# Kernel tuning notes

Hardware: AMD Instinct MI355X
Metric: run time of the kernel (lower is better)

Reference implementation:

```python
import jax, jax.numpy as jnp
import numpy as np

T, B, V, L_MAX = 1000, 64, 1024, 64
BLANK = 0
LAMBDA_FAIR = 0.5
NUM_GROUPS = 2
NEG = jnp.float32(-1e30)  # finite stand-in for -inf (nan-safe under vjp)


def setup_inputs() -> dict:
    key = jax.random.key(0)
    k1, k2, k3, k4, k5 = jax.random.split(key, 5)
    # caller passes log-softmaxed acoustic model outputs [T, B, V]
    log_probs = jax.nn.log_softmax(jax.random.normal(k1, (T, B, V), jnp.float32), axis=-1)
    # flat concatenated targets; values in [1, V) (blank=0 excluded, as in real CTC targets)
    targets = jax.random.randint(k2, (B * L_MAX,), 1, V, dtype=jnp.int32)
    input_lengths = jax.random.randint(k3, (B,), T // 2, T + 1, dtype=jnp.int32)
    target_lengths = jax.random.randint(k4, (B,), 0, L_MAX, dtype=jnp.int32)  # 0 allowed (tests t_len==0 branch)
    group_ids = jax.random.randint(k5, (B,), 0, NUM_GROUPS, dtype=jnp.int32)
    return {"log_probs": log_probs, "targets": targets, "input_lengths": input_lengths,
            "target_lengths": target_lengths, "group_ids": group_ids}


def _ctc_per_sample(log_probs, targets, input_lengths, target_lengths):
    """Batched CTC NLL (reduction='none'), log-domain alpha recursion."""
    Tn, Bn, Vn = log_probs.shape
    # unflatten targets per sample: offsets = exclusive cumsum of target_lengths
    offsets = jnp.cumsum(target_lengths) - target_lengths                      # [B]
    pos = offsets[:, None] + jnp.arange(L_MAX)[None, :]                        # [B, L]
    valid = jnp.arange(L_MAX)[None, :] < target_lengths[:, None]
    tgt = jnp.where(valid, targets[jnp.clip(pos, 0, targets.shape[0] - 1)], BLANK)  # [B, L]

    S = 2 * L_MAX + 1  # extended label sequence with interleaved blanks
    ext = jnp.full((Bn, S), BLANK, dtype=targets.dtype).at[:, 1::2].set(tgt)   # [B, S]
    # emission log-probs gathered once: em[t, b, s] = log_probs[t, b, ext[b, s]]
    em = jnp.take_along_axis(log_probs, jnp.broadcast_to(ext[None], (Tn, Bn, S)), axis=2)

    ext_m2 = jnp.pad(ext[:, :-2], ((0, 0), (2, 0)), constant_values=BLANK)
    s_idx = jnp.arange(S)
    allow_skip = (s_idx[None, :] >= 2) & (ext != BLANK) & (ext != ext_m2)      # [B, S]

    def end_ll(alpha):
        last = 2 * target_lengths                                              # index of final blank
        a1 = jnp.take_along_axis(alpha, last[:, None], axis=1)[:, 0]
        a2 = jnp.take_along_axis(alpha, jnp.clip(last - 1, 0)[:, None], axis=1)[:, 0]
        return jnp.logaddexp(a1, jnp.where(target_lengths > 0, a2, NEG))

    alpha0 = jnp.full((Bn, S), NEG).at[:, 0].set(em[0, :, 0])
    alpha0 = alpha0.at[:, 1].set(jnp.where(target_lengths > 0, em[0, :, 1], NEG))
    final0 = jnp.where(input_lengths == 1, end_ll(alpha0), NEG)

    def step(carry, xs):
        alpha, final = carry
        em_t, t = xs
        sh1 = jnp.concatenate([jnp.full((Bn, 1), NEG), alpha[:, :-1]], axis=1)
        sh2 = jnp.concatenate([jnp.full((Bn, 2), NEG), alpha[:, :-2]], axis=1)
        alpha = jnp.logaddexp(jnp.logaddexp(alpha, sh1),
                              jnp.where(allow_skip, sh2, NEG)) + em_t
        final = jnp.where(t == input_lengths - 1, end_ll(alpha), final)
        return (alpha, final), None

    (_, final), _ = jax.lax.scan(step, (alpha0, final0), (em[1:], jnp.arange(1, Tn)))
    loss = jnp.where(target_lengths > 0, -final, 0.0)   # t_len==0 -> loss 0 (as in original)
    loss = jnp.where(loss < 1e29, loss, 0.0)            # zero_infinity=True
    return loss


def reference(log_probs, targets, input_lengths, target_lengths, group_ids):
    per_sample = _ctc_per_sample(log_probs, targets, input_lengths, target_lengths)  # [B]
    base_loss = per_sample.mean()
    ones = jnp.ones_like(per_sample)
    counts = jax.ops.segment_sum(ones, group_ids, num_segments=NUM_GROUPS)
    sums = jax.ops.segment_sum(per_sample, group_ids, num_segments=NUM_GROUPS)
    group_means = sums / jnp.maximum(counts, 1.0)
    fairness_penalty = jnp.var(group_means, ddof=1)     # torch .var() is unbiased
    total = base_loss + LAMBDA_FAIR * fairness_penalty
    return total, base_loss, fairness_penalty
```

## Files before the change

kernel.cpp:

```cpp
#include <hip/hip_runtime.h>

#define T_ 1000
#define B_ 64
#define V_ 1024
#define LMAX_ 64
#define NEGF (-1e30f)
#define LOG2E_ 1.4426950408889634f
#define LN2_ 0.6931471805599453f
#define P0C 1.4405f
#define P1C (-0.64178f)
#define P2C 0.20128f

__device__ __forceinline__ float ex2(float x) { return __builtin_amdgcn_exp2f(x); }
__device__ __forceinline__ float lg2(float x) { return __builtin_amdgcn_logf(x); }
__device__ __forceinline__ float rlane(float x, int l) {
    return __int_as_float(__builtin_amdgcn_readlane(__float_as_int(x), l));
}
#define FENCE_ __builtin_amdgcn_sched_barrier(0)

__device__ __forceinline__ void load_tgt(const int* __restrict__ targets,
                                         const int* __restrict__ tlen,
                                         int b, int lane, int& tg, int& L) {
    int tl = tlen[lane];
    L = __shfl(tl, b);
    int v = (lane < b) ? tl : 0;
    for (int off = 32; off; off >>= 1) v += __shfl_xor(v, off);
    tg = (lane < L) ? targets[v + lane] : 0;
}

__global__ __launch_bounds__(64) void ctc_fb_k(const float* __restrict__ lp,
                                               const int* __restrict__ targets,
                                               const int* __restrict__ tlen,
                                               const int* __restrict__ ilen,
                                               float* __restrict__ aw) {
    int blk = blockIdx.x, lane = threadIdx.x;
    bool isFwd = blk < B_;
    int b = isFwd ? blk : blk - B_;
    int tg, L;
    load_tgt(targets, tlen, b, lane, tg, L);
    int Tin = ilen[b], Te = Tin - 1;
    int M = Te >> 1;
    int tgp = __shfl_up(tg, 1);
    bool skip1 = (lane >= 1) && (tg != 0) && (tg != tgp);
    int col = (lane == 63) ? 0 : tg;
    int idx = (b << 10) + col;
    float* awb = aw + b * 256;

    if (isFwd) {
        bool is16 = (lane == 16), is32 = (lane == 32), is48 = (lane == 48);
        float a0 = NEGF, a1 = NEGF;
        auto ldG = [&](int g, float4& S) {
            int t0 = 4 * g;
            int ta = t0 < M ? t0 : M, tb2 = t0 + 1 < M ? t0 + 1 : M;
            int tc = t0 + 2 < M ? t0 + 2 : M, td = t0 + 3 < M ? t0 + 3 : M;
            S.x = (lp + ((size_t)ta << 16))[idx];
            S.y = (lp + ((size_t)tb2 << 16))[idx];
            S.z = (lp + ((size_t)tc << 16))[idx];
            S.w = (lp + ((size_t)td << 16))[idx];
        };
        auto shr1 = [&](float x) -> float {
            float v15 = rlane(x, 15), v31 = rlane(x, 31), v47 = rlane(x, 47);
            float bval = is16 ? v15 : (is32 ? v31 : (is48 ? v47 : NEGF));
            return __int_as_float(__builtin_amdgcn_update_dpp(
                __float_as_int(bval), __float_as_int(x), 0x111, 0xF, 0xF, false));
        };
        auto step = [&](float xb, float xe) {
            float p1m = shr1(a1);
            float d0 = a0 - p1m;
            float m0 = fmaxf(a0, p1m);
            float u = ex2(-fabsf(d0));
            float h = fmaf(u, P2C, P1C);
            h = fmaf(u, h, P0C);
            float U = fmaf(u, h, m0);
            float na0 = U + xb;
            float w = skip1 ? U : a0;
            float d1 = a1 - w;
            float m1 = fmaxf(a1, w);
            float v = ex2(-fabsf(d1));
            float h1 = fmaf(v, P2C, P1C);
            h1 = fmaf(v, h1, P0C);
            float na1 = fmaf(v, h1, m1 + xe);
            a0 = na0; a1 = na1;
        };
        if (M >= 35) {
            float4 S0, S1, S2, S3, S4, S5, S6, S7;
            ldG(0, S0); ldG(1, S1); ldG(2, S2); ldG(3, S3);
            ldG(4, S4); ldG(5, S5); ldG(6, S6); ldG(7, S7);
            FENCE_;
            {
                float e0 = S0.x * LOG2E_, e1 = S0.y * LOG2E_;
                float e2 = S0.z * LOG2E_, e3 = S0.w * LOG2E_;
                a0 = (lane == 0) ? rlane(e0, 63) : NEGF;
                a1 = (lane == 0 && L > 0) ? e0 : NEGF;
                step(rlane(e1, 63), e1); step(rlane(e2, 63), e2); step(rlane(e3, 63), e3);
                ldG(8, S0);
                FENCE_;
            }
#define SUBF_F(S, G) do {                                                      \
            float e0_ = S.x * LOG2E_, e1_ = S.y * LOG2E_;                      \
            float e2_ = S.z * LOG2E_, e3_ = S.w * LOG2E_;                      \
            float b0_ = rlane(e0_, 63), b1_ = rlane(e1_, 63);                  \
            float b2_ = rlane(e2_, 63), b3_ = rlane(e3_, 63);                  \
            step(b0_, e0_); step(b1_, e1_); step(b2_, e2_); step(b3_, e3_);    \
            ldG((G) + 8, S);                                                   \
            FENCE_;                                                            \
        } while (0)
            SUBF_F(S1, 1); SUBF_F(S2, 2); SUBF_F(S3, 3); SUBF_F(S4, 4);
            SUBF_F(S5, 5); SUBF_F(S6, 6); SUBF_F(S7, 7);
            int c = 1;
            for (; 32 * c + 31 <= M; ++c) {
                int g0 = 8 * c;
                SUBF_F(S0, g0 + 0); SUBF_F(S1, g0 + 1); SUBF_F(S2, g0 + 2); SUBF_F(S3, g0 + 3);
                SUBF_F(S4, g0 + 4); SUBF_F(S5, g0 + 5); SUBF_F(S6, g0 + 6); SUBF_F(S7, g0 + 7);
            }
#undef SUBF_F
            int tb = 32 * c;
#define SUBT_F(S, T0) do {                                                     \
            float e0_ = S.x * LOG2E_, e1_ = S.y * LOG2E_;                      \
            float e2_ = S.z * LOG2E_, e3_ = S.w * LOG2E_;                      \
            float b0_ = rlane(e0_, 63), b1_ = rlane(e1_, 63);                  \
            float b2_ = rlane(e2_, 63), b3_ = rlane(e3_, 63);                  \
            if ((T0) + 0 <= M) step(b0_, e0_);                                 \
            if ((T0) + 1 <= M) step(b1_, e1_);                                 \
            if ((T0) + 2 <= M) step(b2_, e2_);                                 \
            if ((T0) + 3 <= M) step(b3_, e3_);                                 \
        } while (0)
            SUBT_F(S0, tb + 0);  SUBT_F(S1, tb + 4);  SUBT_F(S2, tb + 8);  SUBT_F(S3, tb + 12);
            SUBT_F(S4, tb + 16); SUBT_F(S5, tb + 20); SUBT_F(S6, tb + 24); SUBT_F(S7, tb + 28);
#undef SUBT_F
        } else {
            float e = lp[idx] * LOG2E_;
            a0 = (lane == 0) ? rlane(e, 63) : NEGF;
            a1 = (lane == 0 && L > 0) ? e : NEGF;
            for (int t = 1; t <= M; ++t) {
                float xe = (lp + ((size_t)t << 16))[idx] * LOG2E_;
                step(rlane(xe, 63), xe);
            }
        }
        awb[lane] = a0;
        awb[64 + lane] = a1;
    } else {
        bool is15 = (lane == 15), is31 = (lane == 31), is47 = (lane == 47);
        int K = Te - M;
        float B0 = (lane == L) ? 0.0f : NEGF;
        float B1 = (L > 0 && lane == L - 1) ? 0.0f : NEGF;
        auto ldG = [&](int g, float4& S) {
            int t0 = Te - 4 * g;
            int ta = t0 > 0 ? t0 : 0, tb2 = t0 - 1 > 0 ? t0 - 1 : 0;
            int tc = t0 - 2 > 0 ? t0 - 2 : 0, td = t0 - 3 > 0 ? t0 - 3 : 0;
            S.x = (lp + ((size_t)ta << 16))[idx];
            S.y = (lp + ((size_t)tb2 << 16))[idx];
            S.z = (lp + ((size_t)tc << 16))[idx];
            S.w = (lp + ((size_t)td << 16))[idx];
        };
        auto shl1 = [&](float x) -> float {
            float v16 = rlane(x, 16), v32 = rlane(x, 32), v48 = rlane(x, 48);
            float bval = is15 ? v16 : (is31 ? v32 : (is47 ? v48 : NEGF));
            return __int_as_float(__builtin_amdgcn_update_dpp(
                __float_as_int(bval), __float_as_int(x), 0x101, 0xF, 0xF, false));
        };
        auto stepb = [&](float xb, float xe) {
            float z = B1 + xe;
            float t0v = B0 + xb;
            float d0 = t0v - z;
            float m0 = fmaxf(t0v, z);
            float u = ex2(-fabsf(d0));
            float h = fmaf(u, P2C, P1C);
            h = fmaf(u, h, P0C);
            float B0n = fmaf(u, h, m0);
            float y = skip1 ? B0n : t0v;
            float arg = shl1(y);
            float d1 = z - arg;
            float m1 = fmaxf(z, arg);
            float v = ex2(-fabsf(d1));
            float h1 = fmaf(v, P2C, P1C);
            h1 = fmaf(v, h1, P0C);
            float B1n = fmaf(v, h1, m1);
            B0 = B0n; B1 = B1n;
        };
        if (K >= 35) {
            float4 S0, S1, S2, S3, S4, S5, S6, S7;
            ldG(0, S0); ldG(1, S1); ldG(2, S2); ldG(3, S3);
            ldG(4, S4); ldG(5, S5); ldG(6, S6); ldG(7, S7);
            FENCE_;
#define SUBF_B(S, G) do {                                                      \
            float e0_ = S.x * LOG2E_, e1_ = S.y * LOG2E_;                      \
            float e2_ = S.z * LOG2E_, e3_ = S.w * LOG2E_;                      \
            float b0_ = rlane(e0_, 63), b1_ = rlane(e1_, 63);                  \
            float b2_ = rlane(e2_, 63), b3_ = rlane(e3_, 63);                  \
            stepb(b0_, e0_); stepb(b1_, e1_); stepb(b2_, e2_); stepb(b3_, e3_);\
            ldG((G) + 8, S);                                                   \
            FENCE_;                                                            \
        } while (0)
            SUBF_B(S0, 0); SUBF_B(S1, 1); SUBF_B(S2, 2); SUBF_B(S3, 3);
            SUBF_B(S4, 4); SUBF_B(S5, 5); SUBF_B(S6, 6); SUBF_B(S7, 7);
            int c = 1;
            for (; 32 * c + 31 <= K - 1; ++c) {
                int g0 = 8 * c;
                SUBF_B(S0, g0 + 0); SUBF_B(S1, g0 + 1); SUBF_B(S2, g0 + 2); SUBF_B(S3, g0 + 3);
                SUBF_B(S4, g0 + 4); SUBF_B(S5, g0 + 5); SUBF_B(S6, g0 + 6); SUBF_B(S7, g0 + 7);
            }
#undef SUBF_B
            int kb = 32 * c;
#define SUBT_B(S, K0) do {                                                     \
            float e0_ = S.x * LOG2E_, e1_ = S.y * LOG2E_;                      \
            float e2_ = S.z * LOG2E_, e3_ = S.w * LOG2E_;                      \
            float b0_ = rlane(e0_, 63), b1_ = rlane(e1_, 63);                  \
            float b2_ = rlane(e2_, 63), b3_ = rlane(e3_, 63);                  \
            if ((K0) + 0 <= K - 1) stepb(b0_, e0_);                            \
            if ((K0) + 1 <= K - 1) stepb(b1_, e1_);                            \
            if ((K0) + 2 <= K - 1) stepb(b2_, e2_);                            \
            if ((K0) + 3 <= K - 1) stepb(b3_, e3_);                            \
        } while (0)
            SUBT_B(S0, kb + 0);  SUBT_B(S1, kb + 4);  SUBT_B(S2, kb + 8);  SUBT_B(S3, kb + 12);
            SUBT_B(S4, kb + 16); SUBT_B(S5, kb + 20); SUBT_B(S6, kb + 24); SUBT_B(S7, kb + 28);
#undef SUBT_B
        } else {
            for (int k = 0; k < K; ++k) {
                int t = Te - k;
                float xe = (lp + ((size_t)t << 16))[idx] * LOG2E_;
                stepb(rlane(xe, 63), xe);
            }
        }
        awb[128 + lane] = B0;
        awb[192 + lane] = B1;
    }
}

__global__ __launch_bounds__(64) void combine_k(const float* __restrict__ aw,
                                                const int* __restrict__ tlen,
                                                const int* __restrict__ ilen,
                                                float* __restrict__ losses) {
    int b = blockIdx.x, lane = threadIdx.x;
    const float* awb = aw + b * 256;
    float s0 = awb[lane] + awb[128 + lane];
    float s1 = awb[64 + lane] + awb[192 + lane];
    float m = fmaxf(s0, s1);
    for (int off = 32; off; off >>= 1) m = fmaxf(m, __shfl_xor(m, off));
    float sum = ex2(s0 - m) + ex2(s1 - m);
    for (int off = 32; off; off >>= 1) sum += __shfl_xor(sum, off);
    if (lane == 0) {
        int L = tlen[b];
        float fin = lg2(sum) + m;
        if (ilen[b] <= 0) fin = NEGF;
        float loss = (L > 0) ? -fin * LN2_ : 0.0f;
        if (!(loss < 1e29f)) loss = 0.0f;
        losses[b] = loss;
    }
}

__global__ __launch_bounds__(64) void ctc_rec_direct_k(const float* __restrict__ lp,
                                                       const int* __restrict__ targets,
                                                       const int* __restrict__ tlen,
                                                       const int* __restrict__ ilen,
                                                       float* __restrict__ losses) {
    int b = blockIdx.x, lane = threadIdx.x;
    int tg, L;
    load_tgt(targets, tlen, b, lane, tg, L);
    int Tin = ilen[b], Te = Tin - 1;
    int tgp = __shfl_up(tg, 1);
    bool skip1 = (lane >= 1) && (tg != 0) && (tg != tgp);
    bool is16 = (lane == 16), is32 = (lane == 32), is48 = (lane == 48);
    int col = (lane == 63) ? 0 : tg;
    int idx = (b << 10) + col;
    float a0 = NEGF, a1 = NEGF;
    auto shr1 = [&](float x) -> float {
        float v15 = rlane(x, 15), v31 = rlane(x, 31), v47 = rlane(x, 47);
        float bval = is16 ? v15 : (is32 ? v31 : (is48 ? v47 : NEGF));
        return __int_as_float(__builtin_amdgcn_update_dpp(
            __float_as_int(bval), __float_as_int(x), 0x111, 0xF, 0xF, false));
    };
    auto step = [&](float xb, float xe) {
        float p1m = shr1(a1);
        float d0 = a0 - p1m;
        float m0 = fmaxf(a0, p1m);
        float u = ex2(-fabsf(d0));
        float h = fmaf(u, P2C, P1C);
        h = fmaf(u, h, P0C);
        float U = fmaf(u, h, m0);
        float na0 = U + xb;
        float w = skip1 ? U : a0;
        float d1 = a1 - w;
        float m1 = fmaxf(a1, w);
        float v = ex2(-fabsf(d1));
        float h1 = fmaf(v, P2C, P1C);
        h1 = fmaf(v, h1, P0C);
        float na1 = fmaf(v, h1, m1 + xe);
        a0 = na0; a1 = na1;
    };
    if (Tin >= 1) {
        float e = lp[idx] * LOG2E_;
        a0 = (lane == 0) ? rlane(e, 63) : NEGF;
        a1 = (lane == 0 && L > 0) ? e : NEGF;
        for (int t = 1; t <= Te; ++t) {
            float xe = (lp + ((size_t)t << 16))[idx] * LOG2E_;
            step(rlane(xe, 63), xe);
        }
    }
    int lidx = (L > 0) ? (L - 1) : 0;
    float aPrev = __shfl(a1, lidx);
    float aLast = __shfl(a0, (L < 63) ? L : 63);
    float x = aLast, y = (L > 0) ? aPrev : NEGF;
    float m = fmaxf(x, y), d = fminf(x, y) - m;
    float fin = m + lg2(1.0f + ex2(d));
    if (Tin <= 0) fin = NEGF;
    if (lane == 0) {
        float loss = (L > 0) ? -fin * LN2_ : 0.0f;
        if (!(loss < 1e29f)) loss = 0.0f;
        losses[b] = loss;
    }
}

__global__ __launch_bounds__(64) void finalize_k(const float* __restrict__ losses,
                                                 const int* __restrict__ gid,
                                                 float* __restrict__ out) {
    int lane = threadIdx.x;
    float l = losses[lane];
    int g = gid[lane];
    float s = l;
    float s0 = (g == 0) ? l : 0.0f, c0 = (g == 0) ? 1.0f : 0.0f;
    float s1 = (g == 1) ? l : 0.0f, c1 = (g == 1) ? 1.0f : 0.0f;
    for (int off = 32; off; off >>= 1) {
        s  += __shfl_xor(s, off);
        s0 += __shfl_xor(s0, off);
        c0 += __shfl_xor(c0, off);
        s1 += __shfl_xor(s1, off);
        c1 += __shfl_xor(c1, off);
    }
    if (lane == 0) {
        float base = s * (1.0f / B_);
        float m0 = s0 / fmaxf(c0, 1.0f);
        float m1 = s1 / fmaxf(c1, 1.0f);
        float mean = 0.5f * (m0 + m1);
        float var = (m0 - mean) * (m0 - mean) + (m1 - mean) * (m1 - mean);
        out[0] = base + 0.5f * var;
        out[1] = base;
        out[2] = var;
    }
}

extern "C" void kernel_launch(void* const* d_in, const int* in_sizes, int n_in,
                              void* d_out, int out_size, void* d_ws, size_t ws_size,
                              hipStream_t stream) {
    const float* lp = (const float*)d_in[0];
    const int* targets = (const int*)d_in[1];
    const int* ilen = (const int*)d_in[2];
    const int* tlen = (const int*)d_in[3];
    const int* gid = (const int*)d_in[4];
    float* out = (float*)d_out;

    char* ws = (char*)d_ws;
    float* losses = (float*)ws;
    float* aw = (float*)(ws + 1024);
    size_t need = 1024 + (size_t)B_ * 256 * 4;

    if (ws_size >= need) {
        ctc_fb_k<<<2 * B_, 64, 0, stream>>>(lp, targets, tlen, ilen, aw);
        combine_k<<<B_, 64, 0, stream>>>(aw, tlen, ilen, losses);
    } else {
        ctc_rec_direct_k<<<B_, 64, 0, stream>>>(lp, targets, tlen, ilen, losses);
    }
    finalize_k<<<1, 64, 0, stream>>>(losses, gid, out);
}
```

Measured before the change: 46.37 us.

## Pre-gather emissions into contiguous float4 buffer and fuse combine with finalize

Adds a highly parallel gather kernel that pulls the needed emission log-probs from the large [T,B,V] tensor, scales them to log2, and writes them into a per-sample, time-packed float4 layout. The serial forward/backward recursion kernels then read one coalesced float4 per lane per four timesteps, instead of four scattered 4-byte loads on the latency-bound critical path. The combine and finalize kernels are merged into one single-block tail kernel to save a launch. The cost is an extra kernel launch plus about 4 MB of workspace writes and reads, and the fast path now needs a larger workspace.

```diff
diff --git a/kernel.cpp b/kernel.cpp
--- a/kernel.cpp
+++ b/kernel.cpp
@@ -1,9 +1,9 @@
 #include <hip/hip_runtime.h>
 
 #define T_ 1000
+#define T4_ 250
 #define B_ 64
 #define V_ 1024
-#define LMAX_ 64
 #define NEGF (-1e30f)
 #define LOG2E_ 1.4426950408889634f
 #define LN2_ 0.6931471805599453f
@@ -28,7 +28,25 @@
     tg = (lane < L) ? targets[v + lane] : 0;
 }
 
-__global__ __launch_bounds__(64) void ctc_fb_k(const float* __restrict__ lp,
+__global__ __launch_bounds__(256) void gather_k(const float* __restrict__ lp,
+                                                const int* __restrict__ targets,
+                                                const int* __restrict__ tlen,
+                                                const int* __restrict__ ilen,
+                                                float* __restrict__ em4f) {
+    int t4 = blockIdx.x % T4_;
+    int b = blockIdx.x / T4_;
+    int tq = threadIdx.x >> 6;
+    int i = threadIdx.x & 63;
+    int tg, L;
+    load_tgt(targets, tlen, b, i, tg, L);
+    int t = t4 * 4 + tq;
+    if (t >= ilen[b]) return;
+    int col = (i == 63) ? 0 : tg;
+    em4f[(((size_t)b * T4_ + t4) * 64 + i) * 4 + tq] =
+        lp[((size_t)t << 16) + (b << 10) + col] * LOG2E_;
+}
+
+__global__ __launch_bounds__(64) void ctc_fb_k(const float4* __restrict__ e44,
                                                const int* __restrict__ targets,
                                                const int* __restrict__ tlen,
                                                const int* __restrict__ ilen,
@@ -42,21 +60,16 @@
     int M = Te >> 1;
     int tgp = __shfl_up(tg, 1);
     bool skip1 = (lane >= 1) && (tg != 0) && (tg != tgp);
-    int col = (lane == 63) ? 0 : tg;
-    int idx = (b << 10) + col;
+    const float4* e44b = e44 + (size_t)b * (T4_ * 64) + lane;
     float* awb = aw + b * 256;
 
     if (isFwd) {
         bool is16 = (lane == 16), is32 = (lane == 32), is48 = (lane == 48);
         float a0 = NEGF, a1 = NEGF;
+        int Gc = M >> 2; if (Gc < 0) Gc = 0;
         auto ldG = [&](int g, float4& S) {
-            int t0 = 4 * g;
-            int ta = t0 < M ? t0 : M, tb2 = t0 + 1 < M ? t0 + 1 : M;
-            int tc = t0 + 2 < M ? t0 + 2 : M, td = t0 + 3 < M ? t0 + 3 : M;
-            S.x = (lp + ((size_t)ta << 16))[idx];
-            S.y = (lp + ((size_t)tb2 << 16))[idx];
-            S.z = (lp + ((size_t)tc << 16))[idx];
-            S.w = (lp + ((size_t)td << 16))[idx];
+            int gm = g < Gc ? g : Gc;
+            S = e44b[(size_t)gm * 64];
         };
         auto shr1 = [&](float x) -> float {
             float v15 = rlane(x, 15), v31 = rlane(x, 31), v47 = rlane(x, 47);
@@ -82,29 +95,19 @@
             float na1 = fmaf(v, h1, m1 + xe);
             a0 = na0; a1 = na1;
         };
+#define STEPF(C) do { float xb_ = rlane((C), 63); step(xb_, (C)); } while (0)
         if (M >= 35) {
             float4 S0, S1, S2, S3, S4, S5, S6, S7;
             ldG(0, S0); ldG(1, S1); ldG(2, S2); ldG(3, S3);
             ldG(4, S4); ldG(5, S5); ldG(6, S6); ldG(7, S7);
             FENCE_;
-            {
-                float e0 = S0.x * LOG2E_, e1 = S0.y * LOG2E_;
-                float e2 = S0.z * LOG2E_, e3 = S0.w * LOG2E_;
-                a0 = (lane == 0) ? rlane(e0, 63) : NEGF;
-                a1 = (lane == 0 && L > 0) ? e0 : NEGF;
-                step(rlane(e1, 63), e1); step(rlane(e2, 63), e2); step(rlane(e3, 63), e3);
-                ldG(8, S0);
-                FENCE_;
-            }
-#define SUBF_F(S, G) do {                                                      \
-            float e0_ = S.x * LOG2E_, e1_ = S.y * LOG2E_;                      \
-            float e2_ = S.z * LOG2E_, e3_ = S.w * LOG2E_;                      \
-            float b0_ = rlane(e0_, 63), b1_ = rlane(e1_, 63);                  \
-            float b2_ = rlane(e2_, 63), b3_ = rlane(e3_, 63);                  \
-            step(b0_, e0_); step(b1_, e1_); step(b2_, e2_); step(b3_, e3_);    \
-            ldG((G) + 8, S);                                                   \
-            FENCE_;                                                            \
-        } while (0)
+            a0 = (lane == 0) ? rlane(S0.x, 63) : NEGF;
+            a1 = (lane == 0 && L > 0) ? S0.x : NEGF;
+            STEPF(S0.y); STEPF(S0.z); STEPF(S0.w);
+            ldG(8, S0);
+            FENCE_;
+#define SUBF_F(S, G) do { STEPF(S.x); STEPF(S.y); STEPF(S.z); STEPF(S.w); \
+                          ldG((G) + 8, S); FENCE_; } while (0)
             SUBF_F(S1, 1); SUBF_F(S2, 2); SUBF_F(S3, 3); SUBF_F(S4, 4);
             SUBF_F(S5, 5); SUBF_F(S6, 6); SUBF_F(S7, 7);
             int c = 1;
@@ -115,28 +118,22 @@
             }
 #undef SUBF_F
             int tb = 32 * c;
-#define SUBT_F(S, T0) do {                                                     \
-            float e0_ = S.x * LOG2E_, e1_ = S.y * LOG2E_;                      \
-            float e2_ = S.z * LOG2E_, e3_ = S.w * LOG2E_;                      \
-            float b0_ = rlane(e0_, 63), b1_ = rlane(e1_, 63);                  \
-            float b2_ = rlane(e2_, 63), b3_ = rlane(e3_, 63);                  \
-            if ((T0) + 0 <= M) step(b0_, e0_);                                 \
-            if ((T0) + 1 <= M) step(b1_, e1_);                                 \
-            if ((T0) + 2 <= M) step(b2_, e2_);                                 \
-            if ((T0) + 3 <= M) step(b3_, e3_);                                 \
-        } while (0)
+#define SUBT_F(S, T0) do { if ((T0) + 0 <= M) STEPF(S.x); if ((T0) + 1 <= M) STEPF(S.y); \
+                           if ((T0) + 2 <= M) STEPF(S.z); if ((T0) + 3 <= M) STEPF(S.w); } while (0)
             SUBT_F(S0, tb + 0);  SUBT_F(S1, tb + 4);  SUBT_F(S2, tb + 8);  SUBT_F(S3, tb + 12);
             SUBT_F(S4, tb + 16); SUBT_F(S5, tb + 20); SUBT_F(S6, tb + 24); SUBT_F(S7, tb + 28);
 #undef SUBT_F
-        } else {
-            float e = lp[idx] * LOG2E_;
+        } else if (Tin >= 1) {
+            const float* emf0 = (const float*)e44b;
+            float e = emf0[0];
             a0 = (lane == 0) ? rlane(e, 63) : NEGF;
             a1 = (lane == 0 && L > 0) ? e : NEGF;
             for (int t = 1; t <= M; ++t) {
-                float xe = (lp + ((size_t)t << 16))[idx] * LOG2E_;
-                step(rlane(xe, 63), xe);
+                float xe = ((const float*)(e44b + (size_t)(t >> 2) * 64))[t & 3];
+                STEPF(xe);
             }
         }
+#undef STEPF
         awb[lane] = a0;
         awb[64 + lane] = a1;
     } else {
@@ -144,15 +141,6 @@
         int K = Te - M;
         float B0 = (lane == L) ? 0.0f : NEGF;
         float B1 = (L > 0 && lane == L - 1) ? 0.0f : NEGF;
-        auto ldG = [&](int g, float4& S) {
-            int t0 = Te - 4 * g;
-            int ta = t0 > 0 ? t0 : 0, tb2 = t0 - 1 > 0 ? t0 - 1 : 0;
-            int tc = t0 - 2 > 0 ? t0 - 2 : 0, td = t0 - 3 > 0 ? t0 - 3 : 0;
-            S.x = (lp + ((size_t)ta << 16))[idx];
-            S.y = (lp + ((size_t)tb2 << 16))[idx];
-            S.z = (lp + ((size_t)tc << 16))[idx];
-            S.w = (lp + ((size_t)td << 16))[idx];
-        };
         auto shl1 = [&](float x) -> float {
             float v16 = rlane(x, 16), v32 = rlane(x, 32), v48 = rlane(x, 48);
             float bval = is15 ? v16 : (is31 ? v32 : (is47 ? v48 : NEGF));
@@ -178,74 +166,102 @@
             float B1n = fmaf(v, h1, m1);
             B0 = B0n; B1 = B1n;
         };
-        if (K >= 35) {
+#define STEPB(C) do { float xb_ = rlane((C), 63); stepb(xb_, (C)); } while (0)
+        if (K >= 40) {
+            int gh = Te >> 2, rP = Te & 3;
+            int KR = K - rP - 1;
+            auto ldGb = [&](int q, float4& S) {
+                int g = gh - 1 - q; if (g < 0) g = 0;
+                S = e44b[(size_t)g * 64];
+            };
+            float4 P = e44b[(size_t)gh * 64];
             float4 S0, S1, S2, S3, S4, S5, S6, S7;
-            ldG(0, S0); ldG(1, S1); ldG(2, S2); ldG(3, S3);
-            ldG(4, S4); ldG(5, S5); ldG(6, S6); ldG(7, S7);
+            ldGb(0, S0); ldGb(1, S1); ldGb(2, S2); ldGb(3, S3);
+            ldGb(4, S4); ldGb(5, S5); ldGb(6, S6); ldGb(7, S7);
             FENCE_;
-#define SUBF_B(S, G) do {                                                      \
-            float e0_ = S.x * LOG2E_, e1_ = S.y * LOG2E_;                      \
-            float e2_ = S.z * LOG2E_, e3_ = S.w * LOG2E_;                      \
-            float b0_ = rlane(e0_, 63), b1_ = rlane(e1_, 63);                  \
-            float b2_ = rlane(e2_, 63), b3_ = rlane(e3_, 63);                  \
-            stepb(b0_, e0_); stepb(b1_, e1_); stepb(b2_, e2_); stepb(b3_, e3_);\
-            ldG((G) + 8, S);                                                   \
-            FENCE_;                                                            \
-        } while (0)
+            if (rP == 3)      { STEPB(P.w); STEPB(P.z); STEPB(P.y); STEPB(P.x); }
+            else if (rP == 2) { STEPB(P.z); STEPB(P.y); STEPB(P.x); }
+            else if (rP == 1) { STEPB(P.y); STEPB(P.x); }
+            else              { STEPB(P.x); }
+#define SUBF_B(S, Q) do { STEPB(S.w); STEPB(S.z); STEPB(S.y); STEPB(S.x); \
+                          ldGb((Q) + 8, S); FENCE_; } while (0)
             SUBF_B(S0, 0); SUBF_B(S1, 1); SUBF_B(S2, 2); SUBF_B(S3, 3);
             SUBF_B(S4, 4); SUBF_B(S5, 5); SUBF_B(S6, 6); SUBF_B(S7, 7);
             int c = 1;
-            for (; 32 * c + 31 <= K - 1; ++c) {
-                int g0 = 8 * c;
-                SUBF_B(S0, g0 + 0); SUBF_B(S1, g0 + 1); SUBF_B(S2, g0 + 2); SUBF_B(S3, g0 + 3);
-                SUBF_B(S4, g0 + 4); SUBF_B(S5, g0 + 5); SUBF_B(S6, g0 + 6); SUBF_B(S7, g0 + 7);
+            for (; 32 * c + 32 <= KR; ++c) {
+                int q0 = 8 * c;
+                SUBF_B(S0, q0 + 0); SUBF_B(S1, q0 + 1); SUBF_B(S2, q0 + 2); SUBF_B(S3, q0 + 3);
+                SUBF_B(S4, q0 + 4); SUBF_B(S5, q0 + 5); SUBF_B(S6, q0 + 6); SUBF_B(S7, q0 + 7);
             }
 #undef SUBF_B
-            int kb = 32 * c;
-#define SUBT_B(S, K0) do {                                                     \
-            float e0_ = S.x * LOG2E_, e1_ = S.y * LOG2E_;                      \
-            float e2_ = S.z * LOG2E_, e3_ = S.w * LOG2E_;                      \
-            float b0_ = rlane(e0_, 63), b1_ = rlane(e1_, 63);                  \
-            float b2_ = rlane(e2_, 63), b3_ = rlane(e3_, 63);                  \
-            if ((K0) + 0 <= K - 1) stepb(b0_, e0_);                            \
-            if ((K0) + 1 <= K - 1) stepb(b1_, e1_);                            \
-            if ((K0) + 2 <= K - 1) stepb(b2_, e2_);                            \
-            if ((K0) + 3 <= K - 1) stepb(b3_, e3_);                            \
-        } while (0)
-            SUBT_B(S0, kb + 0);  SUBT_B(S1, kb + 4);  SUBT_B(S2, kb + 8);  SUBT_B(S3, kb + 12);
-            SUBT_B(S4, kb + 16); SUBT_B(S5, kb + 20); SUBT_B(S6, kb + 24); SUBT_B(S7, kb + 28);
+            int sb = 32 * c;
+#define SUBT_B(S, S0i) do { if ((S0i) + 0 <= KR) STEPB(S.w); if ((S0i) + 1 <= KR) STEPB(S.z); \
+                            if ((S0i) + 2 <= KR) STEPB(S.y); if ((S0i) + 3 <= KR) STEPB(S.x); } while (0)
+            SUBT_B(S0, sb + 1);  SUBT_B(S1, sb + 5);  SUBT_B(S2, sb + 9);  SUBT_B(S3, sb + 13);
+            SUBT_B(S4, sb + 17); SUBT_B(S5, sb + 21); SUBT_B(S6, sb + 25); SUBT_B(S7, sb + 29);
 #undef SUBT_B
         } else {
             for (int k = 0; k < K; ++k) {
                 int t = Te - k;
-                float xe = (lp + ((size_t)t << 16))[idx] * LOG2E_;
-                stepb(rlane(xe, 63), xe);
+                float xe = ((const float*)(e44b + (size_t)(t >> 2) * 64))[t & 3];
+                STEPB(xe);
             }
         }
+#undef STEPB
         awb[128 + lane] = B0;
         awb[192 + lane] = B1;
     }
 }
 
-__global__ __launch_bounds__(64) void combine_k(const float* __restrict__ aw,
-                                                const int* __restrict__ tlen,
-                                                const int* __restrict__ ilen,
-                                                float* __restrict__ losses) {
-    int b = blockIdx.x, lane = threadIdx.x;
-    const float* awb = aw + b * 256;
-    float s0 = awb[lane] + awb[128 + lane];
-    float s1 = awb[64 + lane] + awb[192 + lane];
-    float m = fmaxf(s0, s1);
-    for (int off = 32; off; off >>= 1) m = fmaxf(m, __shfl_xor(m, off));
-    float sum = ex2(s0 - m) + ex2(s1 - m);
-    for (int off = 32; off; off >>= 1) sum += __shfl_xor(sum, off);
-    if (lane == 0) {
-        int L = tlen[b];
-        float fin = lg2(sum) + m;
-        if (ilen[b] <= 0) fin = NEGF;
-        float loss = (L > 0) ? -fin * LN2_ : 0.0f;
-        if (!(loss < 1e29f)) loss = 0.0f;
-        losses[b] = loss;
+__global__ __launch_bounds__(256) void tail_k(const float* __restrict__ aw,
+                                              const int* __restrict__ tlen,
+                                              const int* __restrict__ ilen,
+                                              const int* __restrict__ gid,
+                                              float* __restrict__ out) {
+    __shared__ float lossS[B_];
+    int tid = threadIdx.x, w = tid >> 6, lane = tid & 63;
+    for (int j = 0; j < 16; ++j) {
+        int b = w * 16 + j;
+        const float* awb = aw + b * 256;
+        float s0 = awb[lane] + awb[128 + lane];
+        float s1 = awb[64 + lane] + awb[192 + lane];
+        float m = fmaxf(s0, s1);
+        for (int off = 32; off; off >>= 1) m = fmaxf(m, __shfl_xor(m, off));
+        float sum = ex2(s0 - m) + ex2(s1 - m);
+        for (int off = 32; off; off >>= 1) sum += __shfl_xor(sum, off);
+        if (lane == 0) {
+            int L = tlen[b];
+            float fin = lg2(sum) + m;
+            if (ilen[b] <= 0) fin = NEGF;
+            float loss = (L > 0) ? -fin * LN2_ : 0.0f;
+            if (!(loss < 1e29f)) loss = 0.0f;
+            lossS[b] = loss;
+        }
+    }
+    __syncthreads();
+    if (w == 0) {
+        float l = lossS[lane];
+        int g = gid[lane];
+        float s = l;
+        float s0 = (g == 0) ? l : 0.0f, c0 = (g == 0) ? 1.0f : 0.0f;
+        float s1 = (g == 1) ? l : 0.0f, c1 = (g == 1) ? 1.0f : 0.0f;
+        for (int off = 32; off; off >>= 1) {
+            s  += __shfl_xor(s, off);
+            s0 += __shfl_xor(s0, off);
+            c0 += __shfl_xor(c0, off);
+            s1 += __shfl_xor(s1, off);
+            c1 += __shfl_xor(c1, off);
+        }
+        if (lane == 0) {
+            float base = s * (1.0f / B_);
+            float m0 = s0 / fmaxf(c0, 1.0f);
+            float m1 = s1 / fmaxf(c1, 1.0f);
+            float mean = 0.5f * (m0 + m1);
+            float var = (m0 - mean) * (m0 - mean) + (m1 - mean) * (m1 - mean);
+            out[0] = base + 0.5f * var;
+            out[1] = base;
+            out[2] = var;
+        }
     }
 }
 
@@ -352,13 +368,15 @@
     char* ws = (char*)d_ws;
     float* losses = (float*)ws;
     float* aw = (float*)(ws + 1024);
-    size_t need = 1024 + (size_t)B_ * 256 * 4;
+    float* em4f = (float*)(ws + 131072);
+    size_t need = 131072 + (size_t)B_ * T4_ * 64 * 4 * sizeof(float);
 
     if (ws_size >= need) {
-        ctc_fb_k<<<2 * B_, 64, 0, stream>>>(lp, targets, tlen, ilen, aw);
-        combine_k<<<B_, 64, 0, stream>>>(aw, tlen, ilen, losses);
+        gather_k<<<B_ * T4_, 256, 0, stream>>>(lp, targets, tlen, ilen, em4f);
+        ctc_fb_k<<<2 * B_, 64, 0, stream>>>((const float4*)em4f, targets, tlen, ilen, aw);
+        tail_k<<<1, 256, 0, stream>>>(aw, tlen, ilen, gid, out);
     } else {
         ctc_rec_direct_k<<<B_, 64, 0, stream>>>(lp, targets, tlen, ilen, losses);
-    }
-    finalize_k<<<1, 64, 0, stream>>>(losses, gid, out);
-}
+        finalize_k<<<1, 64, 0, stream>>>(losses, gid, out);
+    }
+}
```

Measured after the change: 71.67 us. +54.6%, slower.

## Stream emissions via global_load_lds ring buffer and use quadratic log1p approximation

Applied to the files above, without the earlier changes.

Replaces the register-held float4 prefetch groups in the forward and backward CTC recursions with a 16-slot LDS ring buffer. The ring is filled by async global_load_lds, with hand-placed vmcnt/lgkmcnt waits and ds_read prefetch four steps ahead. It also shortens the log2(1+2^-x) polynomial from cubic to quadratic, removing one FMA from each of the two dependent chains per step. The aim is to cut register pressure and per-step latency on the serial recursion. The costs are lower accuracy in the logaddexp approximation and fragile inline-asm wait counts.

```diff
diff --git a/kernel.cpp b/kernel.cpp
--- a/kernel.cpp
+++ b/kernel.cpp
@@ -3,13 +3,11 @@
 #define T_ 1000
 #define B_ 64
 #define V_ 1024
-#define LMAX_ 64
 #define NEGF (-1e30f)
 #define LOG2E_ 1.4426950408889634f
 #define LN2_ 0.6931471805599453f
-#define P0C 1.4405f
-#define P1C (-0.64178f)
-#define P2C 0.20128f
+#define C1Q 1.385f
+#define C2Q (-0.385f)
 
 __device__ __forceinline__ float ex2(float x) { return __builtin_amdgcn_exp2f(x); }
 __device__ __forceinline__ float lg2(float x) { return __builtin_amdgcn_logf(x); }
@@ -17,6 +15,12 @@
     return __int_as_float(__builtin_amdgcn_readlane(__float_as_int(x), l));
 }
 #define FENCE_ __builtin_amdgcn_sched_barrier(0)
+
+__device__ __forceinline__ void gload_lds(const float* g, float* l) {
+    __builtin_amdgcn_global_load_lds(
+        (const __attribute__((address_space(1))) unsigned int*)g,
+        (__attribute__((address_space(3))) unsigned int*)l, 4, 0, 0);
+}
 
 __device__ __forceinline__ void load_tgt(const int* __restrict__ targets,
                                          const int* __restrict__ tlen,
@@ -33,6 +37,7 @@
                                                const int* __restrict__ tlen,
                                                const int* __restrict__ ilen,
                                                float* __restrict__ aw) {
+    __shared__ float stg[16][64];
     int blk = blockIdx.x, lane = threadIdx.x;
     bool isFwd = blk < B_;
     int b = isFwd ? blk : blk - B_;
@@ -45,19 +50,19 @@
     int col = (lane == 63) ? 0 : tg;
     int idx = (b << 10) + col;
     float* awb = aw + b * 256;
+    unsigned lbase = (unsigned)(size_t)(__attribute__((address_space(3))) float*)&stg[0][lane];
+
+#define DSRD(R, SLOT) do {                                                     \
+        unsigned la_ = lbase + ((unsigned)(SLOT) << 8);                        \
+        asm volatile("ds_read_b32 %0, %1" : "=v"(R) : "v"(la_));               \
+    } while (0)
+#define WAITV12 do { asm volatile("s_waitcnt vmcnt(12)" ::: "memory"); FENCE_; } while (0)
+#define WAITL3  do { asm volatile("s_waitcnt lgkmcnt(3)" ::: "memory"); FENCE_; } while (0)
+#define DRAIN_  do { asm volatile("s_waitcnt vmcnt(0) lgkmcnt(0)" ::: "memory"); FENCE_; } while (0)
 
     if (isFwd) {
         bool is16 = (lane == 16), is32 = (lane == 32), is48 = (lane == 48);
         float a0 = NEGF, a1 = NEGF;
-        auto ldG = [&](int g, float4& S) {
-            int t0 = 4 * g;
-            int ta = t0 < M ? t0 : M, tb2 = t0 + 1 < M ? t0 + 1 : M;
-            int tc = t0 + 2 < M ? t0 + 2 : M, td = t0 + 3 < M ? t0 + 3 : M;
-            S.x = (lp + ((size_t)ta << 16))[idx];
-            S.y = (lp + ((size_t)tb2 << 16))[idx];
-            S.z = (lp + ((size_t)tc << 16))[idx];
-            S.w = (lp + ((size_t)td << 16))[idx];
-        };
         auto shr1 = [&](float x) -> float {
             float v15 = rlane(x, 15), v31 = rlane(x, 31), v47 = rlane(x, 47);
             float bval = is16 ? v15 : (is32 ? v31 : (is48 ? v47 : NEGF));
@@ -69,66 +74,56 @@
             float d0 = a0 - p1m;
             float m0 = fmaxf(a0, p1m);
             float u = ex2(-fabsf(d0));
-            float h = fmaf(u, P2C, P1C);
-            h = fmaf(u, h, P0C);
+            float h = fmaf(u, C2Q, C1Q);
             float U = fmaf(u, h, m0);
             float na0 = U + xb;
             float w = skip1 ? U : a0;
             float d1 = a1 - w;
             float m1 = fmaxf(a1, w);
             float v = ex2(-fabsf(d1));
-            float h1 = fmaf(v, P2C, P1C);
-            h1 = fmaf(v, h1, P0C);
+            float h1 = fmaf(v, C2Q, C1Q);
             float na1 = fmaf(v, h1, m1 + xe);
             a0 = na0; a1 = na1;
         };
+#define CONSF(R, TT) do {                                                      \
+        WAITL3;                                                                \
+        float e_ = (R) * LOG2E_; float xb_ = rlane(e_, 63); step(xb_, e_);     \
+        int tl_ = (TT) + 16; int tc_ = tl_ < M ? tl_ : M;                      \
+        gload_lds(lp + ((size_t)tc_ << 16) + idx, &stg[(TT) & 15][0]);         \
+        WAITV12;                                                               \
+        DSRD(R, ((TT) + 4) & 15);                                              \
+    } while (0)
         if (M >= 35) {
-            float4 S0, S1, S2, S3, S4, S5, S6, S7;
-            ldG(0, S0); ldG(1, S1); ldG(2, S2); ldG(3, S3);
-            ldG(4, S4); ldG(5, S5); ldG(6, S6); ldG(7, S7);
-            FENCE_;
+            DRAIN_;
+#pragma unroll
+            for (int q = 0; q < 16; ++q) {
+                int tc_ = q < M ? q : M;
+                gload_lds(lp + ((size_t)tc_ << 16) + idx, &stg[q][0]);
+            }
+            WAITV12;
+            float r0, r1, r2, r3;
+            DSRD(r0, 0); DSRD(r1, 1); DSRD(r2, 2); DSRD(r3, 3);
+            WAITL3;
             {
-                float e0 = S0.x * LOG2E_, e1 = S0.y * LOG2E_;
-                float e2 = S0.z * LOG2E_, e3 = S0.w * LOG2E_;
+                float e0 = r0 * LOG2E_;
                 a0 = (lane == 0) ? rlane(e0, 63) : NEGF;
                 a1 = (lane == 0 && L > 0) ? e0 : NEGF;
-                step(rlane(e1, 63), e1); step(rlane(e2, 63), e2); step(rlane(e3, 63), e3);
-                ldG(8, S0);
-                FENCE_;
-            }
-#define SUBF_F(S, G) do {                                                      \
-            float e0_ = S.x * LOG2E_, e1_ = S.y * LOG2E_;                      \
-            float e2_ = S.z * LOG2E_, e3_ = S.w * LOG2E_;                      \
-            float b0_ = rlane(e0_, 63), b1_ = rlane(e1_, 63);                  \
-            float b2_ = rlane(e2_, 63), b3_ = rlane(e3_, 63);                  \
-            step(b0_, e0_); step(b1_, e1_); step(b2_, e2_); step(b3_, e3_);    \
-            ldG((G) + 8, S);                                                   \
-            FENCE_;                                                            \
-        } while (0)
-            SUBF_F(S1, 1); SUBF_F(S2, 2); SUBF_F(S3, 3); SUBF_F(S4, 4);
-            SUBF_F(S5, 5); SUBF_F(S6, 6); SUBF_F(S7, 7);
-            int c = 1;
-            for (; 32 * c + 31 <= M; ++c) {
-                int g0 = 8 * c;
-                SUBF_F(S0, g0 + 0); SUBF_F(S1, g0 + 1); SUBF_F(S2, g0 + 2); SUBF_F(S3, g0 + 3);
-                SUBF_F(S4, g0 + 4); SUBF_F(S5, g0 + 5); SUBF_F(S6, g0 + 6); SUBF_F(S7, g0 + 7);
-            }
-#undef SUBF_F
-            int tb = 32 * c;
-#define SUBT_F(S, T0) do {                                                     \
-            float e0_ = S.x * LOG2E_, e1_ = S.y * LOG2E_;                      \
-            float e2_ = S.z * LOG2E_, e3_ = S.w * LOG2E_;                      \
-            float b0_ = rlane(e0_, 63), b1_ = rlane(e1_, 63);                  \
-            float b2_ = rlane(e2_, 63), b3_ = rlane(e3_, 63);                  \
-            if ((T0) + 0 <= M) step(b0_, e0_);                                 \
-            if ((T0) + 1 <= M) step(b1_, e1_);                                 \
-            if ((T0) + 2 <= M) step(b2_, e2_);                                 \
-            if ((T0) + 3 <= M) step(b3_, e3_);                                 \
-        } while (0)
-            SUBT_F(S0, tb + 0);  SUBT_F(S1, tb + 4);  SUBT_F(S2, tb + 8);  SUBT_F(S3, tb + 12);
-            SUBT_F(S4, tb + 16); SUBT_F(S5, tb + 20); SUBT_F(S6, tb + 24); SUBT_F(S7, tb + 28);
-#undef SUBT_F
-        } else {
+            }
+            {
+                int tc_ = 16 < M ? 16 : M;
+                gload_lds(lp + ((size_t)tc_ << 16) + idx, &stg[0][0]);
+            }
+            WAITV12;
+            DSRD(r0, 4);
+            CONSF(r1, 1); CONSF(r2, 2); CONSF(r3, 3);
+            int t = 4;
+            for (; t + 3 <= M; t += 4) {
+                CONSF(r0, t); CONSF(r1, t + 1); CONSF(r2, t + 2); CONSF(r3, t + 3);
+            }
+            if (t + 0 <= M) CONSF(r0, t + 0);
+            if (t + 1 <= M) CONSF(r1, t + 1);
+            if (t + 2 <= M) CONSF(r2, t + 2);
+        } else if (Tin >= 1) {
             float e = lp[idx] * LOG2E_;
             a0 = (lane == 0) ? rlane(e, 63) : NEGF;
             a1 = (lane == 0 && L > 0) ? e : NEGF;
@@ -137,6 +132,7 @@
                 step(rlane(xe, 63), xe);
             }
         }
+#undef CONSF
         awb[lane] = a0;
         awb[64 + lane] = a1;
     } else {
@@ -144,15 +140,6 @@
         int K = Te - M;
         float B0 = (lane == L) ? 0.0f : NEGF;
         float B1 = (L > 0 && lane == L - 1) ? 0.0f : NEGF;
-        auto ldG = [&](int g, float4& S) {
-            int t0 = Te - 4 * g;
-            int ta = t0 > 0 ? t0 : 0, tb2 = t0 - 1 > 0 ? t0 - 1 : 0;
-            int tc = t0 - 2 > 0 ? t0 - 2 : 0, td = t0 - 3 > 0 ? t0 - 3 : 0;
-            S.x = (lp + ((size_t)ta << 16))[idx];
-            S.y = (lp + ((size_t)tb2 << 16))[idx];
-            S.z = (lp + ((size_t)tc << 16))[idx];
-            S.w = (lp + ((size_t)td << 16))[idx];
-        };
         auto shl1 = [&](float x) -> float {
             float v16 = rlane(x, 16), v32 = rlane(x, 32), v48 = rlane(x, 48);
             float bval = is15 ? v16 : (is31 ? v32 : (is47 ? v48 : NEGF));
@@ -165,56 +152,43 @@
             float d0 = t0v - z;
             float m0 = fmaxf(t0v, z);
             float u = ex2(-fabsf(d0));
-            float h = fmaf(u, P2C, P1C);
-            h = fmaf(u, h, P0C);
+            float h = fmaf(u, C2Q, C1Q);
             float B0n = fmaf(u, h, m0);
             float y = skip1 ? B0n : t0v;
             float arg = shl1(y);
             float d1 = z - arg;
             float m1 = fmaxf(z, arg);
             float v = ex2(-fabsf(d1));
-            float h1 = fmaf(v, P2C, P1C);
-            h1 = fmaf(v, h1, P0C);
+            float h1 = fmaf(v, C2Q, C1Q);
             float B1n = fmaf(v, h1, m1);
             B0 = B0n; B1 = B1n;
         };
+#define CONSB(R, KK) do {                                                      \
+        WAITL3;                                                                \
+        float e_ = (R) * LOG2E_; float xb_ = rlane(e_, 63); stepb(xb_, e_);    \
+        int tl_ = Te - ((KK) + 16); int tc_ = tl_ > 0 ? tl_ : 0;               \
+        gload_lds(lp + ((size_t)tc_ << 16) + idx, &stg[(KK) & 15][0]);         \
+        WAITV12;                                                               \
+        DSRD(R, ((KK) + 4) & 15);                                              \
+    } while (0)
         if (K >= 35) {
-            float4 S0, S1, S2, S3, S4, S5, S6, S7;
-            ldG(0, S0); ldG(1, S1); ldG(2, S2); ldG(3, S3);
-            ldG(4, S4); ldG(5, S5); ldG(6, S6); ldG(7, S7);
-            FENCE_;
-#define SUBF_B(S, G) do {                                                      \
-            float e0_ = S.x * LOG2E_, e1_ = S.y * LOG2E_;                      \
-            float e2_ = S.z * LOG2E_, e3_ = S.w * LOG2E_;                      \
-            float b0_ = rlane(e0_, 63), b1_ = rlane(e1_, 63);                  \
-            float b2_ = rlane(e2_, 63), b3_ = rlane(e3_, 63);                  \
-            stepb(b0_, e0_); stepb(b1_, e1_); stepb(b2_, e2_); stepb(b3_, e3_);\
-            ldG((G) + 8, S);                                                   \
-            FENCE_;                                                            \
-        } while (0)
-            SUBF_B(S0, 0); SUBF_B(S1, 1); SUBF_B(S2, 2); SUBF_B(S3, 3);
-            SUBF_B(S4, 4); SUBF_B(S5, 5); SUBF_B(S6, 6); SUBF_B(S7, 7);
-            int c = 1;
-            for (; 32 * c + 31 <= K - 1; ++c) {
-                int g0 = 8 * c;
-                SUBF_B(S0, g0 + 0); SUBF_B(S1, g0 + 1); SUBF_B(S2, g0 + 2); SUBF_B(S3, g0 + 3);
-                SUBF_B(S4, g0 + 4); SUBF_B(S5, g0 + 5); SUBF_B(S6, g0 + 6); SUBF_B(S7, g0 + 7);
-            }
-#undef SUBF_B
-            int kb = 32 * c;
-#define SUBT_B(S, K0) do {                                                     \
-            float e0_ = S.x * LOG2E_, e1_ = S.y * LOG2E_;                      \
-            float e2_ = S.z * LOG2E_, e3_ = S.w * LOG2E_;                      \
-            float b0_ = rlane(e0_, 63), b1_ = rlane(e1_, 63);                  \
-            float b2_ = rlane(e2_, 63), b3_ = rlane(e3_, 63);                  \
-            if ((K0) + 0 <= K - 1) stepb(b0_, e0_);                            \
-            if ((K0) + 1 <= K - 1) stepb(b1_, e1_);                            \
-            if ((K0) + 2 <= K - 1) stepb(b2_, e2_);                            \
-            if ((K0) + 3 <= K - 1) stepb(b3_, e3_);                            \
-        } while (0)
-            SUBT_B(S0, kb + 0);  SUBT_B(S1, kb + 4);  SUBT_B(S2, kb + 8);  SUBT_B(S3, kb + 12);
-            SUBT_B(S4, kb + 16); SUBT_B(S5, kb + 20); SUBT_B(S6, kb + 24); SUBT_B(S7, kb + 28);
-#undef SUBT_B
+            DRAIN_;
+#pragma unroll
+            for (int q = 0; q < 16; ++q) {
+                int tl_ = Te - q; int tc_ = tl_ > 0 ? tl_ : 0;
+                gload_lds(lp + ((size_t)tc_ << 16) + idx, &stg[q][0]);
+            }
+            WAITV12;
+            float r0, r1, r2, r3;
+            DSRD(r0, 0); DSRD(r1, 1); DSRD(r2, 2); DSRD(r3, 3);
+            CONSB(r0, 0); CONSB(r1, 1); CONSB(r2, 2); CONSB(r3, 3);
+            int k = 4;
+            for (; k + 3 <= K - 1; k += 4) {
+                CONSB(r0, k); CONSB(r1, k + 1); CONSB(r2, k + 2); CONSB(r3, k + 3);
+            }
+            if (k + 0 <= K - 1) CONSB(r0, k + 0);
+            if (k + 1 <= K - 1) CONSB(r1, k + 1);
+            if (k + 2 <= K - 1) CONSB(r2, k + 2);
         } else {
             for (int k = 0; k < K; ++k) {
                 int t = Te - k;
@@ -222,9 +196,14 @@
                 stepb(rlane(xe, 63), xe);
             }
         }
+#undef CONSB
         awb[128 + lane] = B0;
         awb[192 + lane] = B1;
     }
+#undef DSRD
+#undef WAITV12
+#undef WAITL3
+#undef DRAIN_
 }
 
 __global__ __launch_bounds__(64) void combine_k(const float* __restrict__ aw,
@@ -275,16 +254,14 @@
         float d0 = a0 - p1m;
         float m0 = fmaxf(a0, p1m);
         float u = ex2(-fabsf(d0));
-        float h = fmaf(u, P2C, P1C);
-        h = fmaf(u, h, P0C);
+        float h = fmaf(u, C2Q, C1Q);
         float U = fmaf(u, h, m0);
         float na0 = U + xb;
         float w = skip1 ? U : a0;
         float d1 = a1 - w;
         float m1 = fmaxf(a1, w);
         float v = ex2(-fabsf(d1));
-        float h1 = fmaf(v, P2C, P1C);
-        h1 = fmaf(v, h1, P0C);
+        float h1 = fmaf(v, C2Q, C1Q);
         float na1 = fmaf(v, h1, m1 + xe);
         a0 = na0; a1 = na1;
     };
```

Result: slower. 55.21 us (+19.1%).
